# Kernel tuning notes

Measured on AMD Instinct MI355X. Metric: run time of the kernel, lower is better.

The kernel has to match this reference:

```python
import jax, jax.numpy as jnp
import numpy as np

DIM = 1024
HEADS = 16
DIM_HEAD = 64
INNER = HEADS * DIM_HEAD  # 1024
SCALE = DIM_HEAD ** -0.5


def setup_inputs() -> dict:
    key = jax.random.key(0)
    k_x, k_qkv, k_ow, k_ob = jax.random.split(key, 4)
    B, N = 4, 2048
    x = jax.random.normal(k_x, (B, N, DIM), dtype=jnp.float32)
    # nn.Linear weights stored as [out, in] in torch; keep [in, out] for x @ W.
    w_qkv = jax.random.normal(k_qkv, (DIM, 3 * INNER), dtype=jnp.float32) * (DIM ** -0.5)
    w_out = jax.random.normal(k_ow, (INNER, DIM), dtype=jnp.float32) * (INNER ** -0.5)
    b_out = jax.random.normal(k_ob, (DIM,), dtype=jnp.float32) * 0.01
    return {"x": x, "w_qkv": w_qkv, "w_out": w_out, "b_out": b_out}


def reference(x, w_qkv, w_out, b_out):
    B, N, _ = x.shape
    qkv = x @ w_qkv  # [B, N, 3*inner]
    q, k, v = jnp.split(qkv, 3, axis=-1)
    # [B, N, inner] -> [B, H, N, dh]
    def to_heads(t):
        return t.reshape(B, N, HEADS, DIM_HEAD).transpose(0, 2, 1, 3)
    q, k, v = to_heads(q), to_heads(k), to_heads(v)
    attn = jnp.einsum("bhqd,bhkd->bhqk", q, k) * SCALE  # [B, H, N, N]
    attn = jax.nn.softmax(attn, axis=-1)
    out = jnp.einsum("bhqk,bhkd->bhqd", attn, v)  # [B, H, N, dh]
    out = out.transpose(0, 2, 1, 3).reshape(B, N, INNER)
    return out @ w_out + b_out
```

## Files before the change

kernel.cpp:

```cpp
#include <hip/hip_runtime.h>
#include <hip/hip_bf16.h>
#include <stdint.h>

typedef __attribute__((ext_vector_type(4))) float f32x4;
typedef __attribute__((ext_vector_type(16))) float f32x16;
typedef __attribute__((ext_vector_type(8))) short s16x8;
typedef __attribute__((ext_vector_type(4))) short s16x4;
typedef __attribute__((ext_vector_type(4))) unsigned int u32x4;

#define DEV static __device__ __forceinline__

constexpr int B_ = 4, H_ = 16, N_ = 2048;
constexpr float CL_ = 0.18033688011112042f;

DEV short f2bf(float x) {
  __hip_bfloat16 h = __float2bfloat16(x);
  return *reinterpret_cast<short*>(&h);
}

DEV uint32_t cvtpk(float lo, float hi) {
  uint32_t r;
  asm("v_cvt_pk_bf16_f32 %0, %1, %2" : "=v"(r) : "v"(lo), "v"(hi));
  return r;
}

DEV void gload16(const void* g, void* l) {
  __builtin_amdgcn_global_load_lds((const __attribute__((address_space(1))) void*)g,
                                   (__attribute__((address_space(3))) void*)l, 16, 0, 0);
}

__global__ void k_prep(const float* __restrict__ x, short* __restrict__ xb,
                       const float* __restrict__ wqkv, short* __restrict__ wqkvT,
                       const float* __restrict__ wout, short* __restrict__ woutT) {
  __shared__ short t[64][72];
  int bid = blockIdx.x, tid = threadIdx.x;
  if (bid < 4096) {
    int i = (bid * 256 + tid) * 8;
    const float4* p = reinterpret_cast<const float4*>(x + i);
    float4 a = p[0], b = p[1];
    s16x8 o;
    o[0] = f2bf(a.x); o[1] = f2bf(a.y); o[2] = f2bf(a.z); o[3] = f2bf(a.w);
    o[4] = f2bf(b.x); o[5] = f2bf(b.y); o[6] = f2bf(b.z); o[7] = f2bf(b.w);
    *reinterpret_cast<s16x8*>(xb + i) = o;
    return;
  }
  const float* W;
  short* WT;
  int R = 1024, C, r0, c0;
  if (bid < 4864) {
    int id = bid - 4096;
    W = wqkv; WT = wqkvT; C = 3072;
    c0 = (id % 48) * 64; r0 = (id / 48) * 64;
  } else {
    int id = bid - 4864;
    W = wout; WT = woutT; C = 1024;
    c0 = (id % 16) * 64; r0 = (id / 16) * 64;
  }
  int r = tid >> 2, cp = (tid & 3) * 16;
  const float4* s4 = reinterpret_cast<const float4*>(W + (size_t)(r0 + r) * C + c0 + cp);
  float4 f0 = s4[0], f1 = s4[1], f2 = s4[2], f3 = s4[3];
  short* tr = &t[r][cp];
  tr[0] = f2bf(f0.x); tr[1] = f2bf(f0.y); tr[2]  = f2bf(f0.z); tr[3]  = f2bf(f0.w);
  tr[4] = f2bf(f1.x); tr[5] = f2bf(f1.y); tr[6]  = f2bf(f1.z); tr[7]  = f2bf(f1.w);
  tr[8] = f2bf(f2.x); tr[9] = f2bf(f2.y); tr[10] = f2bf(f2.z); tr[11] = f2bf(f2.w);
  tr[12] = f2bf(f3.x); tr[13] = f2bf(f3.y); tr[14] = f2bf(f3.z); tr[15] = f2bf(f3.w);
  __syncthreads();
  int cc = tid >> 2, rp = (tid & 3) * 16;
  short buf[16];
#pragma unroll
  for (int i = 0; i < 16; ++i) buf[i] = t[rp + i][cc];
  short* dst = WT + (size_t)(c0 + cc) * R + r0 + rp;
  *reinterpret_cast<s16x8*>(dst) = *reinterpret_cast<s16x8*>(buf);
  *reinterpret_cast<s16x8*>(dst + 8) = *reinterpret_cast<s16x8*>(buf + 8);
}

__global__ __launch_bounds__(256, 2)
void k_gemm0(const short* __restrict__ A, const short* __restrict__ BT,
             short* __restrict__ oq, short* __restrict__ ok, short* __restrict__ ovT) {
  __shared__ __align__(16) char smem[32768];
  constexpr int K = 1024, NT = 32;
  const int tid = threadIdx.x;
  const int m0 = blockIdx.x * 128, n0 = blockIdx.y * 128;
  const int lane = tid & 63, w = tid >> 6, g = lane >> 4, c = lane & 15;
  const int wr = w >> 1, wc = w & 1;
  f32x4 acc[4][4] = {};
  const int trow = tid >> 2, tk = (tid & 3) * 8;
  const short* ga = A + (size_t)(m0 + trow) * K + tk;
  const short* gb = BT + (size_t)(n0 + trow) * K + tk;
#define STG0(T)                                                    \
  {                                                                \
    char* nb = smem + ((T) & 1) * 16384;                           \
    gload16(ga + (T) * 32, nb + tid * 16);                         \
    gload16(ga + (size_t)64 * K + (T) * 32, nb + 4096 + tid * 16); \
    gload16(gb + (T) * 32, nb + 8192 + tid * 16);                  \
    gload16(gb + (size_t)64 * K + (T) * 32, nb + 12288 + tid * 16);\
  }
  STG0(0);
  asm volatile("s_waitcnt vmcnt(0)" ::: "memory");
  __builtin_amdgcn_s_barrier();
  for (int t = 0; t < NT; ++t) {
    if (t + 1 < NT) STG0(t + 1);
    const char* sb = smem + (t & 1) * 16384;
    s16x8 af[4], bf[4];
#pragma unroll
    for (int i = 0; i < 4; ++i)
      af[i] = *reinterpret_cast<const s16x8*>(sb + (wr * 64 + i * 16 + c) * 64 + g * 16);
#pragma unroll
    for (int j = 0; j < 4; ++j)
      bf[j] = *reinterpret_cast<const s16x8*>(sb + 8192 + (wc * 64 + j * 16 + c) * 64 + g * 16);
    __builtin_amdgcn_s_setprio(1);
#pragma unroll
    for (int i = 0; i < 4; ++i)
#pragma unroll
      for (int j = 0; j < 4; ++j)
        acc[i][j] = __builtin_amdgcn_mfma_f32_16x16x32_bf16(af[i], bf[j], acc[i][j], 0, 0, 0);
    __builtin_amdgcn_s_setprio(0);
    asm volatile("s_waitcnt vmcnt(0)" ::: "memory");
    __builtin_amdgcn_s_barrier();
  }
#undef STG0
#pragma unroll
  for (int bj = 0; bj < 4; ++bj) {
    int ncol = n0 + wc * 64 + bj * 16 + c;
    int part = ncol >> 10;
    int c10 = ncol & 1023;
    int h = c10 >> 6, d = c10 & 63;
    if (part == 2) {
#pragma unroll
      for (int ai = 0; ai < 4; ++ai) {
        int mrow = m0 + wr * 64 + ai * 16 + g * 4;
        int b = mrow >> 11, nr = mrow & 2047;
        uint2 pk;
        pk.x = cvtpk(acc[ai][bj][0], acc[ai][bj][1]);
        pk.y = cvtpk(acc[ai][bj][2], acc[ai][bj][3]);
        *reinterpret_cast<uint2*>(ovT + ((size_t)((b * H_ + h) * 64 + d) * N_ + nr)) = pk;
      }
    } else {
      short* dst0 = (part == 0) ? oq : ok;
      float qs = (part == 0) ? CL_ : 1.0f;
#pragma unroll
      for (int ai = 0; ai < 4; ++ai) {
#pragma unroll
        for (int r = 0; r < 4; ++r) {
          int mrow = m0 + wr * 64 + ai * 16 + g * 4 + r;
          int b = mrow >> 11, nr = mrow & 2047;
          dst0[((size_t)((b * H_ + h) * N_ + nr) << 6) + d] = f2bf(acc[ai][bj][r] * qs);
        }
      }
    }
  }
}

__global__ __launch_bounds__(256, 2)
void k_gemm1(const short* __restrict__ A, const short* __restrict__ BT,
             int M, int N, int K, const float* __restrict__ bias, float* __restrict__ out) {
  __shared__ __align__(16) char smem[65536];
  const int NT = K / 64;
  const int tid = threadIdx.x;
  const int m0 = blockIdx.x * 128, n0 = blockIdx.y * 128;
  const int lane = tid & 63, w = tid >> 6, g = lane >> 4, c = lane & 15;
  const int wr = w >> 1, wc = w & 1;
  f32x4 acc[4][4] = {};
  int ci0 = tid, ci1 = tid + 256, ci2 = tid + 512, ci3 = tid + 768;
  int r0_ = ci0 >> 3, r1_ = ci1 >> 3, r2_ = ci2 >> 3, r3_ = ci3 >> 3;
  int sc0 = ((ci0 & 7) ^ ((r0_ ^ (r0_ >> 3)) & 7)) * 8;
  int sc1 = ((ci1 & 7) ^ ((r1_ ^ (r1_ >> 3)) & 7)) * 8;
  int sc2 = ((ci2 & 7) ^ ((r2_ ^ (r2_ >> 3)) & 7)) * 8;
  int sc3 = ((ci3 & 7) ^ ((r3_ ^ (r3_ >> 3)) & 7)) * 8;
  const short* ga0 = A + (size_t)(m0 + r0_) * K + sc0;
  const short* ga1 = A + (size_t)(m0 + r1_) * K + sc1;
  const short* ga2 = A + (size_t)(m0 + r2_) * K + sc2;
  const short* ga3 = A + (size_t)(m0 + r3_) * K + sc3;
  const short* gb0 = BT + (size_t)(n0 + r0_) * K + sc0;
  const short* gb1 = BT + (size_t)(n0 + r1_) * K + sc1;
  const short* gb2 = BT + (size_t)(n0 + r2_) * K + sc2;
  const short* gb3 = BT + (size_t)(n0 + r3_) * K + sc3;
#define STG1(T)                                                      \
  {                                                                  \
    char* nb = smem + ((T) & 1) * 32768;                             \
    gload16(ga0 + (T) * 64, nb + ci0 * 16);                          \
    gload16(ga1 + (T) * 64, nb + ci1 * 16);                          \
    gload16(ga2 + (T) * 64, nb + ci2 * 16);                          \
    gload16(ga3 + (T) * 64, nb + ci3 * 16);                          \
    gload16(gb0 + (T) * 64, nb + 16384 + ci0 * 16);                  \
    gload16(gb1 + (T) * 64, nb + 16384 + ci1 * 16);                  \
    gload16(gb2 + (T) * 64, nb + 16384 + ci2 * 16);                  \
    gload16(gb3 + (T) * 64, nb + 16384 + ci3 * 16);                  \
  }
  int offA[4][2], offB[4][2];
#pragma unroll
  for (int i = 0; i < 4; ++i) {
    int ra = wr * 64 + i * 16 + c;
    int sa = (ra ^ (ra >> 3)) & 7;
    int rb = wc * 64 + i * 16 + c;
    int sb2 = (rb ^ (rb >> 3)) & 7;
#pragma unroll
    for (int ks = 0; ks < 2; ++ks) {
      offA[i][ks] = ra * 128 + (((ks * 4 + g) ^ sa) * 16);
      offB[i][ks] = 16384 + rb * 128 + (((ks * 4 + g) ^ sb2) * 16);
    }
  }
  STG1(0);
  asm volatile("s_waitcnt vmcnt(0)" ::: "memory");
  __builtin_amdgcn_s_barrier();
  for (int t = 0; t < NT; ++t) {
    if (t + 1 < NT) STG1(t + 1);
    const char* sb = smem + (t & 1) * 32768;
#pragma unroll
    for (int ks = 0; ks < 2; ++ks) {
      s16x8 af[4], bf[4];
#pragma unroll
      for (int i = 0; i < 4; ++i)
        af[i] = *reinterpret_cast<const s16x8*>(sb + offA[i][ks]);
#pragma unroll
      for (int j = 0; j < 4; ++j)
        bf[j] = *reinterpret_cast<const s16x8*>(sb + offB[j][ks]);
      __builtin_amdgcn_s_setprio(1);
#pragma unroll
      for (int i = 0; i < 4; ++i)
#pragma unroll
        for (int j = 0; j < 4; ++j)
          acc[i][j] = __builtin_amdgcn_mfma_f32_16x16x32_bf16(af[i], bf[j], acc[i][j], 0, 0, 0);
      __builtin_amdgcn_s_setprio(0);
    }
    asm volatile("s_waitcnt vmcnt(0)" ::: "memory");
    __builtin_amdgcn_s_barrier();
  }
#undef STG1
#pragma unroll
  for (int bj = 0; bj < 4; ++bj) {
    int ncol = n0 + wc * 64 + bj * 16 + c;
    float bb = bias[ncol];
#pragma unroll
    for (int ai = 0; ai < 4; ++ai) {
#pragma unroll
      for (int r = 0; r < 4; ++r) {
        int mrow = m0 + wr * 64 + ai * 16 + g * 4 + r;
        out[(size_t)mrow * N + ncol] = acc[ai][bj][r] + bb;
      }
    }
  }
}

__global__ __launch_bounds__(256, 4)
void k_attn(const short* __restrict__ q, const short* __restrict__ kk,
            const short* __restrict__ vT, short* __restrict__ ao) {
  __shared__ __align__(16) char smem[32768];
  constexpr int NT = N_ / 64;
  int bh = blockIdx.x, qb = blockIdx.y;
  int b = bh >> 4, head = bh & 15;
  int tid = threadIdx.x, w = tid >> 6, lane = tid & 63;
  int half = lane >> 5, qc = lane & 31;
  const size_t ho = (size_t)bh * (N_ * 64);
  const short* Q = q + ho;
  const char* Kc = reinterpret_cast<const char*>(kk + ho);
  const char* Vc = reinterpret_cast<const char*>(vT + ho);
  int q0w = qb * 128 + w * 32;
  s16x8 qf[4];
#pragma unroll
  for (int ks = 0; ks < 4; ++ks)
    qf[ks] = *reinterpret_cast<const s16x8*>(Q + (size_t)(q0w + qc) * 64 + ks * 16 + half * 8);
  f32x16 ot[2] = {};
  float lp0 = 0.f, lp1 = 0.f, lp2 = 0.f, lp3 = 0.f;
  const int rsw0 = ((qc ^ (qc >> 3)) & 7) << 4;
  const int rsw1 = rsw0 ^ 0x40;
  const int s_i0 = tid, s_i1 = tid + 256;
  const int s_r0 = s_i0 >> 3, s_r1 = s_i1 >> 3;
  const int s_c0 = (((s_i0 & 7) ^ ((s_r0 ^ (s_r0 >> 3)) & 7)) << 4);
  const int s_c1 = (((s_i1 & 7) ^ ((s_r1 ^ (s_r1 >> 3)) & 7)) << 4);
#define STAGE(T)                                                                       \
  {                                                                                    \
    char* nb = smem + ((T) & 1) * 16384;                                               \
    gload16(Kc + (size_t)((T) * 64 + s_r0) * 128 + s_c0, nb + s_i0 * 16);              \
    gload16(Kc + (size_t)((T) * 64 + s_r1) * 128 + s_c1, nb + s_i1 * 16);              \
    gload16(Vc + (size_t)s_r0 * 4096 + (T) * 128 + s_c0, nb + 8192 + s_i0 * 16);       \
    gload16(Vc + (size_t)s_r1 * 4096 + (T) * 128 + s_c1, nb + 8192 + s_i1 * 16);       \
  }
  STAGE(0);
  __syncthreads();
  for (int tt = 0; tt < NT; ++tt) {
    if (tt + 1 < NT) STAGE(tt + 1);
    const char* kb_ = smem + (tt & 1) * 16384;
    const char* vb_ = kb_ + 8192;
    f32x16 st[2];
#pragma unroll
    for (int j = 0; j < 2; ++j) {
      const int rs = j ? rsw1 : rsw0;
      s16x8 kfj[4];
#pragma unroll
      for (int ks = 0; ks < 4; ++ks)
        kfj[ks] = *reinterpret_cast<const s16x8*>(kb_ + (j * 32 + qc) * 128 + ((ks * 32 + half * 16) ^ rs));
      f32x16 acc = {};
      __builtin_amdgcn_s_setprio(1);
#pragma unroll
      for (int ks = 0; ks < 4; ++ks)
        acc = __builtin_amdgcn_mfma_f32_32x32x16_bf16(kfj[ks], qf[ks], acc, 0, 0, 0);
      __builtin_amdgcn_s_setprio(0);
      st[j] = acc;
    }
#pragma unroll
    for (int j = 0; j < 2; ++j)
#pragma unroll
      for (int r = 0; r < 16; ++r) {
        float p = __builtin_amdgcn_exp2f(st[j][r]);
        st[j][r] = p;
        if ((r & 3) == 0) lp0 += p;
        else if ((r & 3) == 1) lp1 += p;
        else if ((r & 3) == 2) lp2 += p;
        else lp3 += p;
      }
    u32x4 pwv[4];
#pragma unroll
    for (int j = 0; j < 2; ++j)
#pragma unroll
      for (int bb = 0; bb < 2; ++bb)
#pragma unroll
        for (int p = 0; p < 2; ++p) {
          uint32_t Aw = cvtpk(st[j][8 * bb + 2 * p], st[j][8 * bb + 2 * p + 1]);
          uint32_t Bw = cvtpk(st[j][8 * bb + 4 + 2 * p], st[j][8 * bb + 4 + 2 * p + 1]);
          asm volatile("v_permlane32_swap_b32 %0, %1" : "+v"(Aw), "+v"(Bw));
          pwv[j * 2 + bb][p] = Aw;
          pwv[j * 2 + bb][p + 2] = Bw;
        }
#pragma unroll
    for (int db = 0; db < 2; ++db) {
      const int rs = db ? rsw1 : rsw0;
      s16x8 vf[4];
#pragma unroll
      for (int kb4 = 0; kb4 < 4; ++kb4)
        vf[kb4] = *reinterpret_cast<const s16x8*>(vb_ + (db * 32 + qc) * 128 + ((kb4 * 32 + half * 16) ^ rs));
      f32x16 acc = ot[db];
      __builtin_amdgcn_s_setprio(1);
#pragma unroll
      for (int kb4 = 0; kb4 < 4; ++kb4)
        acc = __builtin_amdgcn_mfma_f32_32x32x16_bf16(
            vf[kb4], __builtin_bit_cast(s16x8, pwv[kb4]), acc, 0, 0, 0);
      __builtin_amdgcn_s_setprio(0);
      ot[db] = acc;
    }
    __syncthreads();
  }
#undef STAGE
  float lp = (lp0 + lp1) + (lp2 + lp3);
  float linv = 1.f / (lp + __shfl_xor(lp, 32, 64));
  short* Oq = reinterpret_cast<short*>(smem) + w * 2304;
#pragma unroll
  for (int db = 0; db < 2; ++db)
#pragma unroll
    for (int m = 0; m < 4; ++m) {
      uint2 pk;
      pk.x = cvtpk(ot[db][4 * m] * linv, ot[db][4 * m + 1] * linv);
      pk.y = cvtpk(ot[db][4 * m + 2] * linv, ot[db][4 * m + 3] * linv);
      *reinterpret_cast<uint2*>(Oq + qc * 72 + db * 32 + m * 8 + half * 4) = pk;
    }
  int q2 = lane >> 1, dcol = (lane & 1) * 32;
  size_t ro = (size_t)(b * N_ + q0w + q2) * 1024 + head * 64 + dcol;
#pragma unroll
  for (int ch = 0; ch < 4; ++ch) {
    s16x8 vv = *reinterpret_cast<const s16x8*>(Oq + q2 * 72 + dcol + ch * 8);
    *reinterpret_cast<s16x8*>(ao + ro + ch * 8) = vv;
  }
}

extern "C" void kernel_launch(void* const* d_in, const int* in_sizes, int n_in,
                              void* d_out, int out_size, void* d_ws, size_t ws_size,
                              hipStream_t stream) {
  const float* x = (const float*)d_in[0];
  const float* w_qkv = (const float*)d_in[1];
  const float* w_out = (const float*)d_in[2];
  const float* b_out = (const float*)d_in[3];
  float* out = (float*)d_out;
  char* ws = (char*)d_ws;
  short* xb    = (short*)(ws);
  short* wqkvT = (short*)(ws + 16777216);
  short* woutT = (short*)(ws + 23068672);
  short* qB    = (short*)(ws + 25165824);
  short* kB    = (short*)(ws + 41943040);
  short* vTT   = (short*)(ws + 75497472);
  short* ao    = xb;

  k_prep<<<5120, 256, 0, stream>>>(x, xb, w_qkv, wqkvT, w_out, woutT);
  k_gemm0<<<dim3(64, 24), 256, 0, stream>>>(xb, wqkvT, qB, kB, vTT);
  k_attn<<<dim3(64, 16), 256, 0, stream>>>(qB, kB, vTT, ao);
  k_gemm1<<<dim3(64, 8), 256, 0, stream>>>(ao, woutT, 8192, 1024, 1024, b_out, out);
}
```

Measured before the change: 186.3 us.

## Double K-tile depth in QKV GEMM and add XOR-swizzled LDS layout

The QKV projection GEMM now stages 64-wide K tiles instead of 32-wide, which halves the number of loop iterations and barriers. Shared memory grows to 64KB of double buffer. Global-to-LDS loads use an XOR swizzle on the 16-byte chunk index, and the fragment reads use the matching swizzled offsets, so 128-byte LDS rows do not cause bank conflicts. The larger LDS footprint may limit occupancy to the two blocks per CU set in the launch bounds, and it raises the per-stage load latency that has to be hidden.

```diff
diff --git a/kernel.cpp b/kernel.cpp
--- a/kernel.cpp
+++ b/kernel.cpp
@@ -77,44 +77,75 @@
 __global__ __launch_bounds__(256, 2)
 void k_gemm0(const short* __restrict__ A, const short* __restrict__ BT,
              short* __restrict__ oq, short* __restrict__ ok, short* __restrict__ ovT) {
-  __shared__ __align__(16) char smem[32768];
-  constexpr int K = 1024, NT = 32;
+  __shared__ __align__(16) char smem[65536];
+  constexpr int K = 1024, NT = 16;
   const int tid = threadIdx.x;
   const int m0 = blockIdx.x * 128, n0 = blockIdx.y * 128;
   const int lane = tid & 63, w = tid >> 6, g = lane >> 4, c = lane & 15;
   const int wr = w >> 1, wc = w & 1;
   f32x4 acc[4][4] = {};
-  const int trow = tid >> 2, tk = (tid & 3) * 8;
-  const short* ga = A + (size_t)(m0 + trow) * K + tk;
-  const short* gb = BT + (size_t)(n0 + trow) * K + tk;
-#define STG0(T)                                                    \
-  {                                                                \
-    char* nb = smem + ((T) & 1) * 16384;                           \
-    gload16(ga + (T) * 32, nb + tid * 16);                         \
-    gload16(ga + (size_t)64 * K + (T) * 32, nb + 4096 + tid * 16); \
-    gload16(gb + (T) * 32, nb + 8192 + tid * 16);                  \
-    gload16(gb + (size_t)64 * K + (T) * 32, nb + 12288 + tid * 16);\
+  int ci0 = tid, ci1 = tid + 256, ci2 = tid + 512, ci3 = tid + 768;
+  int r0_ = ci0 >> 3, r1_ = ci1 >> 3, r2_ = ci2 >> 3, r3_ = ci3 >> 3;
+  int sc0 = ((ci0 & 7) ^ ((r0_ ^ (r0_ >> 3)) & 7)) * 8;
+  int sc1 = ((ci1 & 7) ^ ((r1_ ^ (r1_ >> 3)) & 7)) * 8;
+  int sc2 = ((ci2 & 7) ^ ((r2_ ^ (r2_ >> 3)) & 7)) * 8;
+  int sc3 = ((ci3 & 7) ^ ((r3_ ^ (r3_ >> 3)) & 7)) * 8;
+  const short* ga0 = A + (size_t)(m0 + r0_) * K + sc0;
+  const short* ga1 = A + (size_t)(m0 + r1_) * K + sc1;
+  const short* ga2 = A + (size_t)(m0 + r2_) * K + sc2;
+  const short* ga3 = A + (size_t)(m0 + r3_) * K + sc3;
+  const short* gb0 = BT + (size_t)(n0 + r0_) * K + sc0;
+  const short* gb1 = BT + (size_t)(n0 + r1_) * K + sc1;
+  const short* gb2 = BT + (size_t)(n0 + r2_) * K + sc2;
+  const short* gb3 = BT + (size_t)(n0 + r3_) * K + sc3;
+#define STG0(T)                                                      \
+  {                                                                  \
+    char* nb = smem + ((T) & 1) * 32768;                             \
+    gload16(ga0 + (T) * 64, nb + ci0 * 16);                          \
+    gload16(ga1 + (T) * 64, nb + ci1 * 16);                          \
+    gload16(ga2 + (T) * 64, nb + ci2 * 16);                          \
+    gload16(ga3 + (T) * 64, nb + ci3 * 16);                          \
+    gload16(gb0 + (T) * 64, nb + 16384 + ci0 * 16);                  \
+    gload16(gb1 + (T) * 64, nb + 16384 + ci1 * 16);                  \
+    gload16(gb2 + (T) * 64, nb + 16384 + ci2 * 16);                  \
+    gload16(gb3 + (T) * 64, nb + 16384 + ci3 * 16);                  \
+  }
+  int offA[4][2], offB[4][2];
+#pragma unroll
+  for (int i = 0; i < 4; ++i) {
+    int ra = wr * 64 + i * 16 + c;
+    int sa = (ra ^ (ra >> 3)) & 7;
+    int rb = wc * 64 + i * 16 + c;
+    int sb2 = (rb ^ (rb >> 3)) & 7;
+#pragma unroll
+    for (int ks = 0; ks < 2; ++ks) {
+      offA[i][ks] = ra * 128 + (((ks * 4 + g) ^ sa) * 16);
+      offB[i][ks] = 16384 + rb * 128 + (((ks * 4 + g) ^ sb2) * 16);
+    }
   }
   STG0(0);
   asm volatile("s_waitcnt vmcnt(0)" ::: "memory");
   __builtin_amdgcn_s_barrier();
   for (int t = 0; t < NT; ++t) {
     if (t + 1 < NT) STG0(t + 1);
-    const char* sb = smem + (t & 1) * 16384;
-    s16x8 af[4], bf[4];
-#pragma unroll
-    for (int i = 0; i < 4; ++i)
-      af[i] = *reinterpret_cast<const s16x8*>(sb + (wr * 64 + i * 16 + c) * 64 + g * 16);
-#pragma unroll
-    for (int j = 0; j < 4; ++j)
-      bf[j] = *reinterpret_cast<const s16x8*>(sb + 8192 + (wc * 64 + j * 16 + c) * 64 + g * 16);
-    __builtin_amdgcn_s_setprio(1);
-#pragma unroll
-    for (int i = 0; i < 4; ++i)
+    const char* sb = smem + (t & 1) * 32768;
+#pragma unroll
+    for (int ks = 0; ks < 2; ++ks) {
+      s16x8 af[4], bf[4];
+#pragma unroll
+      for (int i = 0; i < 4; ++i)
+        af[i] = *reinterpret_cast<const s16x8*>(sb + offA[i][ks]);
 #pragma unroll
       for (int j = 0; j < 4; ++j)
-        acc[i][j] = __builtin_amdgcn_mfma_f32_16x16x32_bf16(af[i], bf[j], acc[i][j], 0, 0, 0);
-    __builtin_amdgcn_s_setprio(0);
+        bf[j] = *reinterpret_cast<const s16x8*>(sb + offB[j][ks]);
+      __builtin_amdgcn_s_setprio(1);
+#pragma unroll
+      for (int i = 0; i < 4; ++i)
+#pragma unroll
+        for (int j = 0; j < 4; ++j)
+          acc[i][j] = __builtin_amdgcn_mfma_f32_16x16x32_bf16(af[i], bf[j], acc[i][j], 0, 0, 0);
+      __builtin_amdgcn_s_setprio(0);
+    }
     asm volatile("s_waitcnt vmcnt(0)" ::: "memory");
     __builtin_amdgcn_s_barrier();
   }
```

New measurement: 177.0 us. -5.0%, faster.
